# Kernel tuning notes

Hardware: AMD Instinct MI355X
Metric: run time of the kernel (lower is better)

Reference implementation:

```python
import jax, jax.numpy as jnp
import numpy as np

NEG = -1.0e9

def setup_inputs() -> dict:
    key = jax.random.key(0)
    k1, k2 = jax.random.split(key)
    B, S, D = 4, 4096, 256
    encodings = jax.random.normal(k1, (B, S, D), dtype=jnp.float32)
    # nn.Linear weight [out, in]; Linear applies x @ W.T
    W = jax.random.normal(k2, (D, D), dtype=jnp.float32) * (1.0 / np.sqrt(D))
    return {"encodings": encodings, "W": W}

def reference(encodings, W):
    B, S, D = encodings.shape
    enc_mult_W = jnp.einsum('bsd,ed->bse', encodings, W)          # Linear, no bias
    sims = jnp.einsum('bqd,bkd->bqk', encodings, enc_mult_W)       # E @ (EW^T)^T
    scaled = sims / jnp.asarray(np.sqrt(D), dtype=sims.dtype)
    # causal mask: positions k > q masked out (top-left softmax == 1)
    mask = jnp.triu(jnp.ones((S, S), dtype=bool), k=1)
    scaled = jnp.where(mask[None, :, :], jnp.asarray(NEG, scaled.dtype), scaled)
    attn = jax.nn.softmax(scaled, axis=-1)
    return jnp.einsum('bqk,bkd->bqd', attn, encodings)
```

## Files before the change

### kernel.cpp

```cpp
#include <hip/hip_runtime.h>
#include <hip/hip_bf16.h>
#include <cstdint>
#include <cstddef>

typedef __attribute__((ext_vector_type(4))) float f32x4;
typedef __attribute__((ext_vector_type(8))) short s16x8;
typedef __attribute__((ext_vector_type(4))) unsigned int u32x4;

#define SDIM 4096
#define DDIM 256

#define GLOAD_LDS16(g, s)                                                      \
  __builtin_amdgcn_global_load_lds(                                            \
      (const __attribute__((address_space(1))) void*)(g),                      \
      (__attribute__((address_space(3))) void*)(s), 16, 0, 0)

__device__ __forceinline__ unsigned short cvt_bf16(float f) {
  union { float f; unsigned int u; } v;
  v.f = f;
  unsigned int u = v.u;
  unsigned int r = (u + 0x7FFFu + ((u >> 16) & 1u)) >> 16;
  return (unsigned short)r;
}

__device__ __forceinline__ float bf2f(unsigned short s) {
  union { unsigned int u; float f; } v;
  v.u = ((unsigned int)s) << 16;
  return v.f;
}

__global__ __launch_bounds__(256) void k_convw(const float* __restrict__ W,
                                               unsigned short* __restrict__ Wb) {
  int i = (blockIdx.x * 256 + threadIdx.x) * 8;
  f32x4 a = *(const f32x4*)(W + i);
  f32x4 b = *(const f32x4*)(W + i + 4);
  s16x8 o;
#pragma unroll
  for (int j = 0; j < 4; ++j) {
    o[j] = (short)cvt_bf16(a[j]);
    o[4 + j] = (short)cvt_bf16(b[j]);
  }
  *(s16x8*)(Wb + i) = o;
}

__global__ __launch_bounds__(256) void k_transv(const float* __restrict__ E,
                                                unsigned short* __restrict__ Vt) {
  __shared__ float tile[64][65];
  const int tid = threadIdx.x;
  const int b = blockIdx.z;
  const int s0 = blockIdx.x * 64, d0 = blockIdx.y * 64;
  const int tx = tid & 63, ty = tid >> 6;
#pragma unroll
  for (int i = 0; i < 16; ++i) {
    int sr = i * 4 + ty;
    tile[sr][tx] = E[((size_t)(b * SDIM) + s0 + sr) * DDIM + d0 + tx];
  }
  __syncthreads();
#pragma unroll
  for (int i = 0; i < 16; ++i) {
    int dr = i * 4 + ty;
    Vt[((size_t)(b * DDIM) + d0 + dr) * SDIM + s0 + tx] = cvt_bf16(tile[tx][dr]);
  }
}

__global__ __launch_bounds__(256) void k_proj(const float* __restrict__ E,
                                              const unsigned short* __restrict__ Wb,
                                              unsigned short* __restrict__ Kp) {
  const int tid = threadIdx.x;
  const int w = tid >> 6, l = tid & 63, lhi = l >> 4, llo = l & 15;
  const int m0 = blockIdx.x * 64 + w * 16;
  f32x4 acc[16];
#pragma unroll
  for (int n = 0; n < 16; ++n) acc[n] = (f32x4){0.f, 0.f, 0.f, 0.f};
  const float* arow = E + (size_t)(m0 + llo) * DDIM;
#pragma unroll
  for (int kd = 0; kd < 8; ++kd) {
    const int dbase = kd * 32 + lhi * 8;
    f32x4 a0 = *(const f32x4*)(arow + dbase);
    f32x4 a1 = *(const f32x4*)(arow + dbase + 4);
    s16x8 af;
#pragma unroll
    for (int j = 0; j < 4; ++j) {
      af[j] = (short)cvt_bf16(a0[j]);
      af[4 + j] = (short)cvt_bf16(a1[j]);
    }
#pragma unroll
    for (int n = 0; n < 16; ++n) {
      s16x8 bf = *(const s16x8*)(Wb + (n * 16 + llo) * DDIM + dbase);
      acc[n] = __builtin_amdgcn_mfma_f32_16x16x32_bf16(af, bf, acc[n], 0, 0, 0);
    }
  }
  const float sc = 1.4426950408889634f / 16.0f;
#pragma unroll
  for (int n = 0; n < 16; ++n) {
#pragma unroll
    for (int r = 0; r < 4; ++r) {
      Kp[(size_t)(m0 + lhi * 4 + r) * DDIM + n * 16 + llo] = cvt_bf16(acc[n][r] * sc);
    }
  }
}

__global__ __launch_bounds__(256, 2) void k_attn(const float* __restrict__ E,
                                                 const unsigned short* __restrict__ Kp,
                                                 const unsigned short* __restrict__ Vt,
                                                 unsigned short* __restrict__ Po,
                                                 float* __restrict__ Lp, int nch) {
  __shared__ u32x4 smem4[4736];
  char* smem = (char*)smem4;
  const int tid = threadIdx.x;
  const int l = tid & 63, w = tid >> 6, lhi = l >> 4, llo = l & 15;
  const int u = blockIdx.x % (4 * nch);
  const int t_ = blockIdx.x / (4 * nch);
  const int qt = 31 - t_;
  const int b = u & 3, ch = u >> 2;
  const int q0 = qt * 128;
  const int chb = ch * 4 + b;
  const int nst = (4 * (qt + 1) - ch + nch - 1) / nch;
  const int wq0 = q0 + w * 32;

  if (4 * (qt + 1) <= ch) {
    char* Pz = (char*)(Po + ((size_t)chb * SDIM + q0) * DDIM);
    const u32x4 z = (u32x4){0u, 0u, 0u, 0u};
#pragma unroll
    for (int i = 0; i < 16; ++i) *(u32x4*)(Pz + tid * 256 + i * 16) = z;
    if (tid < 128) Lp[(size_t)chb * SDIM + q0 + tid] = 0.f;
    return;
  }

  s16x8 qf[2][8];
#pragma unroll
  for (int s = 0; s < 2; ++s) {
    const float* Eq = E + ((size_t)(b * SDIM) + wq0 + s * 16 + llo) * DDIM;
#pragma unroll
    for (int kd = 0; kd < 8; ++kd) {
      f32x4 a0 = *(const f32x4*)(Eq + kd * 32 + lhi * 8);
      f32x4 a1 = *(const f32x4*)(Eq + kd * 32 + lhi * 8 + 4);
#pragma unroll
      for (int j = 0; j < 4; ++j) {
        qf[s][kd][j] = (short)cvt_bf16(a0[j]);
        qf[s][kd][4 + j] = (short)cvt_bf16(a1[j]);
      }
    }
  }

  f32x4 oT[2][16];
#pragma unroll
  for (int s = 0; s < 2; ++s)
#pragma unroll
    for (int n = 0; n < 16; ++n) oT[s][n] = (f32x4){0.f, 0.f, 0.f, 0.f};
  float lsum[2] = {0.f, 0.f};

  const int trow = tid >> 5;
  const int kcolb = ((tid & 31) << 4) ^ ((trow & 7) << 4);
  const char* KpB = (const char*)Kp + (size_t)b * SDIM * 512;
  const char* VtB = (const char*)Vt + (size_t)b * DDIM * (SDIM * 2);
  const char* vsb = VtB + (size_t)(tid >> 2) * 8192 + (size_t)((tid & 3) * 8) * 2;

  auto stage = [&](int t) {
    const int kv0 = (ch + nch * t) * 32;
    char* kdst = smem + ((t & 1) * 16384);
    char* vdst = smem + 32768 + ((t & 1) * 16384);
    const char* ks = KpB + (size_t)(kv0 + trow) * 512 + kcolb;
    const char* vs = vsb + (size_t)kv0 * 2;
#pragma unroll
    for (int i = 0; i < 4; ++i)
      GLOAD_LDS16(ks + (size_t)i * 4096, kdst + i * 4096 + tid * 16);
#pragma unroll
    for (int i = 0; i < 4; ++i)
      GLOAD_LDS16(vs + (size_t)i * (64 * 8192), vdst + i * 4096 + tid * 16);
  };

  stage(0);
  char* sPw = smem + 65536 + w * 2560;

  for (int t = 0; t < nst; ++t) {
    const int kv0 = (ch + nch * t) * 32;
    const char* kb_ = smem + ((t & 1) * 16384);
    const char* vb_ = smem + 32768 + ((t & 1) * 16384);

    __syncthreads();
    if (t + 1 < nst) stage(t + 1);

#pragma unroll
    for (int kb = 0; kb < 2; ++kb) {
      f32x4 sa0 = (f32x4){0.f, 0.f, 0.f, 0.f};
      f32x4 sa1 = (f32x4){0.f, 0.f, 0.f, 0.f};
      const char* krow = kb_ + (kb * 16 + llo) * 512;
      __builtin_amdgcn_s_setprio(1);
#pragma unroll
      for (int kd = 0; kd < 8; ++kd) {
        s16x8 kf = *(const s16x8*)(krow + ((kd * 64 + lhi * 16) ^ ((llo & 7) << 4)));
        sa0 = __builtin_amdgcn_mfma_f32_16x16x32_bf16(kf, qf[0][kd], sa0, 0, 0, 0);
        sa1 = __builtin_amdgcn_mfma_f32_16x16x32_bf16(kf, qf[1][kd], sa1, 0, 0, 0);
      }
      __builtin_amdgcn_s_setprio(0);
      const int kvr = kv0 + kb * 16 + lhi * 4;
#pragma unroll
      for (int s = 0; s < 2; ++s) {
        const f32x4 sa = s ? sa1 : sa0;
        const int qi = wq0 + s * 16 + llo;
        float p[4];
#pragma unroll
        for (int rr = 0; rr < 4; ++rr) {
          float v = exp2f(sa[rr] - 32.0f);
          p[rr] = (kvr + rr > qi) ? 0.0f : v;
        }
        lsum[s] += (p[0] + p[1]) + (p[2] + p[3]);
        unsigned int w0 = __builtin_amdgcn_perm(__float_as_uint(p[1]),
                                                __float_as_uint(p[0]), 0x07060302u);
        unsigned int w1 = __builtin_amdgcn_perm(__float_as_uint(p[3]),
                                                __float_as_uint(p[2]), 0x07060302u);
        *(uint2*)(sPw + (s * 16 + llo) * 80 + kb * 32 + lhi * 8) = make_uint2(w0, w1);
      }
    }

    s16x8 pb0 = *(const s16x8*)(sPw + llo * 80 + lhi * 16);
    s16x8 pb1 = *(const s16x8*)(sPw + (16 + llo) * 80 + lhi * 16);
    __builtin_amdgcn_s_setprio(1);
#pragma unroll
    for (int n = 0; n < 16; ++n) {
      s16x8 vf = *(const s16x8*)(vb_ + (n * 16 + llo) * 64 + lhi * 16);
      oT[0][n] = __builtin_amdgcn_mfma_f32_16x16x32_bf16(vf, pb0, oT[0][n], 0, 0, 0);
      oT[1][n] = __builtin_amdgcn_mfma_f32_16x16x32_bf16(vf, pb1, oT[1][n], 0, 0, 0);
    }
    __builtin_amdgcn_s_setprio(0);
  }

#pragma unroll
  for (int s = 0; s < 2; ++s) {
    lsum[s] += __shfl_xor(lsum[s], 16);
    lsum[s] += __shfl_xor(lsum[s], 32);
  }
#pragma unroll
  for (int s = 0; s < 2; ++s) {
    const int q = wq0 + s * 16 + llo;
    unsigned short* PoW = Po + ((size_t)chb * SDIM + q) * DDIM;
#pragma unroll
    for (int n = 0; n < 16; ++n) {
      unsigned int w0 =
          (unsigned int)cvt_bf16(oT[s][n][0]) | ((unsigned int)cvt_bf16(oT[s][n][1]) << 16);
      unsigned int w1 =
          (unsigned int)cvt_bf16(oT[s][n][2]) | ((unsigned int)cvt_bf16(oT[s][n][3]) << 16);
      *(uint2*)(PoW + n * 16 + lhi * 4) = make_uint2(w0, w1);
    }
    if (lhi == 0) Lp[(size_t)chb * SDIM + q] = lsum[s];
  }
}

__global__ __launch_bounds__(256) void k_merge(const unsigned short* __restrict__ Po,
                                               const float* __restrict__ Lp,
                                               float* __restrict__ out, int nch) {
  const size_t e = ((size_t)blockIdx.x * 256 + threadIdx.x) * 8;
  const size_t f = e >> 8;
  float lt = 0.f;
  for (int c = 0; c < nch; ++c) lt += Lp[(size_t)c * 16384 + f];
  const float inv = 1.0f / lt;
  float acc[8] = {0.f, 0.f, 0.f, 0.f, 0.f, 0.f, 0.f, 0.f};
  for (int c = 0; c < nch; ++c) {
    s16x8 a = *(const s16x8*)(Po + (size_t)c * 4194304 + e);
#pragma unroll
    for (int j = 0; j < 8; ++j) acc[j] += bf2f((unsigned short)a[j]);
  }
  f32x4 o0, o1;
#pragma unroll
  for (int j = 0; j < 4; ++j) {
    o0[j] = acc[j] * inv;
    o1[j] = acc[4 + j] * inv;
  }
  *(f32x4*)(out + e) = o0;
  *(f32x4*)(out + e + 4) = o1;
}

extern "C" void kernel_launch(void* const* d_in, const int* in_sizes, int n_in,
                              void* d_out, int out_size, void* d_ws, size_t ws_size,
                              hipStream_t stream) {
  (void)in_sizes; (void)n_in; (void)out_size;
  const float* E = (const float*)d_in[0];
  const float* W = (const float*)d_in[1];
  float* out = (float*)d_out;
  char* ws = (char*)d_ws;

  const size_t base = 16777216ull;
  auto need = [&](int c) {
    return base + (size_t)c * 8388608ull + (size_t)c * 65536ull + 262144ull;
  };
  int nch = 2;
  if (ws_size >= need(8)) nch = 8;
  else if (ws_size >= need(4)) nch = 4;

  unsigned short* Kp = (unsigned short*)(ws);
  unsigned short* Vt = (unsigned short*)(ws + 8388608);
  unsigned short* Po = (unsigned short*)(ws + base);
  size_t lp_off = base + (size_t)nch * 8388608ull;
  float* Lp = (float*)(ws + lp_off);
  unsigned short* Wb = (unsigned short*)(ws + lp_off + (size_t)nch * 65536ull);

  k_convw<<<dim3(32), dim3(256), 0, stream>>>(W, Wb);
  k_transv<<<dim3(64, 4, 4), dim3(256), 0, stream>>>(E, Vt);
  k_proj<<<dim3(256), dim3(256), 0, stream>>>(E, Wb, Kp);
  k_attn<<<dim3(32 * 4 * nch), dim3(256), 0, stream>>>(E, Kp, Vt, Po, Lp, nch);
  k_merge<<<dim3(2048), dim3(256), 0, stream>>>(Po, Lp, out, nch);
}
```

Measured before the change: 126.3 us.

## Use 64-key tiles, read V from global, skip empty chunks, merge prep kernels

Fuses the W conversion and V transpose into one prep kernel, saving a launch. The attention kernel now processes 64-key tiles with only K staged through LDS, while V fragments are read directly from global memory. The P scratch layout is swizzled, and the causal mask is applied only on diagonal tiles. Chunks with no work return early instead of writing zeros, and the merge kernel sums only the chunks that could be valid. This cuts zero-fill traffic, merge reads and LDS traffic, at the cost of uncoalesced global V loads and bigger LDS use, which may lower occupancy.

```diff
diff --git a/kernel.cpp b/kernel.cpp
--- a/kernel.cpp
+++ b/kernel.cpp
@@ -29,26 +29,28 @@
   return v.f;
 }
 
-__global__ __launch_bounds__(256) void k_convw(const float* __restrict__ W,
-                                               unsigned short* __restrict__ Wb) {
-  int i = (blockIdx.x * 256 + threadIdx.x) * 8;
-  f32x4 a = *(const f32x4*)(W + i);
-  f32x4 b = *(const f32x4*)(W + i + 4);
-  s16x8 o;
-#pragma unroll
-  for (int j = 0; j < 4; ++j) {
-    o[j] = (short)cvt_bf16(a[j]);
-    o[4 + j] = (short)cvt_bf16(b[j]);
-  }
-  *(s16x8*)(Wb + i) = o;
-}
-
-__global__ __launch_bounds__(256) void k_transv(const float* __restrict__ E,
-                                                unsigned short* __restrict__ Vt) {
+__global__ __launch_bounds__(256) void k_prep(const float* __restrict__ E,
+                                              const float* __restrict__ W,
+                                              unsigned short* __restrict__ Wb,
+                                              unsigned short* __restrict__ Vt) {
   __shared__ float tile[64][65];
+  const int bid = blockIdx.x;
   const int tid = threadIdx.x;
-  const int b = blockIdx.z;
-  const int s0 = blockIdx.x * 64, d0 = blockIdx.y * 64;
+  if (bid >= 1024) {
+    int i = ((bid - 1024) * 256 + tid) * 8;
+    f32x4 a = *(const f32x4*)(W + i);
+    f32x4 b = *(const f32x4*)(W + i + 4);
+    s16x8 o;
+#pragma unroll
+    for (int j = 0; j < 4; ++j) {
+      o[j] = (short)cvt_bf16(a[j]);
+      o[4 + j] = (short)cvt_bf16(b[j]);
+    }
+    *(s16x8*)(Wb + i) = o;
+    return;
+  }
+  const int b = bid >> 8;
+  const int d0 = ((bid >> 6) & 3) * 64, s0 = (bid & 63) * 64;
   const int tx = tid & 63, ty = tid >> 6;
 #pragma unroll
   for (int i = 0; i < 16; ++i) {
@@ -105,7 +107,7 @@
                                                  const unsigned short* __restrict__ Vt,
                                                  unsigned short* __restrict__ Po,
                                                  float* __restrict__ Lp, int nch) {
-  __shared__ u32x4 smem4[4736];
+  __shared__ u32x4 smem4[5120];
   char* smem = (char*)smem4;
   const int tid = threadIdx.x;
   const int l = tid & 63, w = tid >> 6, lhi = l >> 4, llo = l & 15;
@@ -115,17 +117,10 @@
   const int b = u & 3, ch = u >> 2;
   const int q0 = qt * 128;
   const int chb = ch * 4 + b;
-  const int nst = (4 * (qt + 1) - ch + nch - 1) / nch;
+  const int ntile = 2 * (qt + 1);
+  if (ntile <= ch) return;
+  const int nst = (ntile - ch + nch - 1) / nch;
   const int wq0 = q0 + w * 32;
-
-  if (4 * (qt + 1) <= ch) {
-    char* Pz = (char*)(Po + ((size_t)chb * SDIM + q0) * DDIM);
-    const u32x4 z = (u32x4){0u, 0u, 0u, 0u};
-#pragma unroll
-    for (int i = 0; i < 16; ++i) *(u32x4*)(Pz + tid * 256 + i * 16) = z;
-    if (tid < 128) Lp[(size_t)chb * SDIM + q0 + tid] = 0.f;
-    return;
-  }
 
   s16x8 qf[2][8];
 #pragma unroll
@@ -154,35 +149,31 @@
   const int kcolb = ((tid & 31) << 4) ^ ((trow & 7) << 4);
   const char* KpB = (const char*)Kp + (size_t)b * SDIM * 512;
   const char* VtB = (const char*)Vt + (size_t)b * DDIM * (SDIM * 2);
-  const char* vsb = VtB + (size_t)(tid >> 2) * 8192 + (size_t)((tid & 3) * 8) * 2;
+  const char* vbase = VtB + (size_t)llo * 8192 + lhi * 16;
 
   auto stage = [&](int t) {
-    const int kv0 = (ch + nch * t) * 32;
-    char* kdst = smem + ((t & 1) * 16384);
-    char* vdst = smem + 32768 + ((t & 1) * 16384);
+    const int kv0 = (ch + nch * t) * 64;
+    char* kdst = smem + ((t & 1) * 32768);
     const char* ks = KpB + (size_t)(kv0 + trow) * 512 + kcolb;
-    const char* vs = vsb + (size_t)kv0 * 2;
-#pragma unroll
-    for (int i = 0; i < 4; ++i)
+#pragma unroll
+    for (int i = 0; i < 8; ++i)
       GLOAD_LDS16(ks + (size_t)i * 4096, kdst + i * 4096 + tid * 16);
-#pragma unroll
-    for (int i = 0; i < 4; ++i)
-      GLOAD_LDS16(vs + (size_t)i * (64 * 8192), vdst + i * 4096 + tid * 16);
   };
 
   stage(0);
-  char* sPw = smem + 65536 + w * 2560;
+  char* sPw = smem + 65536 + w * 4096;
+  const int prd = (llo & 3) << 5;
 
   for (int t = 0; t < nst; ++t) {
-    const int kv0 = (ch + nch * t) * 32;
-    const char* kb_ = smem + ((t & 1) * 16384);
-    const char* vb_ = smem + 32768 + ((t & 1) * 16384);
+    const int kv0 = (ch + nch * t) * 64;
+    const char* kb_ = smem + ((t & 1) * 32768);
 
     __syncthreads();
     if (t + 1 < nst) stage(t + 1);
 
-#pragma unroll
-    for (int kb = 0; kb < 2; ++kb) {
+    const bool diag = (kv0 + 64 > q0);
+#pragma unroll
+    for (int kb = 0; kb < 4; ++kb) {
       f32x4 sa0 = (f32x4){0.f, 0.f, 0.f, 0.f};
       f32x4 sa1 = (f32x4){0.f, 0.f, 0.f, 0.f};
       const char* krow = kb_ + (kb * 16 + llo) * 512;
@@ -198,30 +189,42 @@
 #pragma unroll
       for (int s = 0; s < 2; ++s) {
         const f32x4 sa = s ? sa1 : sa0;
-        const int qi = wq0 + s * 16 + llo;
         float p[4];
 #pragma unroll
-        for (int rr = 0; rr < 4; ++rr) {
-          float v = exp2f(sa[rr] - 32.0f);
-          p[rr] = (kvr + rr > qi) ? 0.0f : v;
+        for (int rr = 0; rr < 4; ++rr) p[rr] = exp2f(sa[rr] - 32.0f);
+        if (diag) {
+          const int qi = wq0 + s * 16 + llo;
+#pragma unroll
+          for (int rr = 0; rr < 4; ++rr)
+            if (kvr + rr > qi) p[rr] = 0.0f;
         }
         lsum[s] += (p[0] + p[1]) + (p[2] + p[3]);
         unsigned int w0 = __builtin_amdgcn_perm(__float_as_uint(p[1]),
                                                 __float_as_uint(p[0]), 0x07060302u);
         unsigned int w1 = __builtin_amdgcn_perm(__float_as_uint(p[3]),
                                                 __float_as_uint(p[2]), 0x07060302u);
-        *(uint2*)(sPw + (s * 16 + llo) * 80 + kb * 32 + lhi * 8) = make_uint2(w0, w1);
+        const int r = s * 16 + llo;
+        *(uint2*)(sPw + r * 128 + ((kb * 32 + lhi * 8) ^ ((r & 3) << 5))) =
+            make_uint2(w0, w1);
       }
     }
 
-    s16x8 pb0 = *(const s16x8*)(sPw + llo * 80 + lhi * 16);
-    s16x8 pb1 = *(const s16x8*)(sPw + (16 + llo) * 80 + lhi * 16);
+    s16x8 pb[2][2];
+#pragma unroll
+    for (int ks = 0; ks < 2; ++ks) {
+      pb[0][ks] = *(const s16x8*)(sPw + llo * 128 + ((ks * 64 + lhi * 16) ^ prd));
+      pb[1][ks] = *(const s16x8*)(sPw + (16 + llo) * 128 + ((ks * 64 + lhi * 16) ^ prd));
+    }
+    const char* vt0 = vbase + (size_t)kv0 * 2;
     __builtin_amdgcn_s_setprio(1);
 #pragma unroll
     for (int n = 0; n < 16; ++n) {
-      s16x8 vf = *(const s16x8*)(vb_ + (n * 16 + llo) * 64 + lhi * 16);
-      oT[0][n] = __builtin_amdgcn_mfma_f32_16x16x32_bf16(vf, pb0, oT[0][n], 0, 0, 0);
-      oT[1][n] = __builtin_amdgcn_mfma_f32_16x16x32_bf16(vf, pb1, oT[1][n], 0, 0, 0);
+#pragma unroll
+      for (int ks = 0; ks < 2; ++ks) {
+        s16x8 vf = *(const s16x8*)(vt0 + (size_t)n * 131072 + ks * 64);
+        oT[0][n] = __builtin_amdgcn_mfma_f32_16x16x32_bf16(vf, pb[0][ks], oT[0][n], 0, 0, 0);
+        oT[1][n] = __builtin_amdgcn_mfma_f32_16x16x32_bf16(vf, pb[1][ks], oT[1][n], 0, 0, 0);
+      }
     }
     __builtin_amdgcn_s_setprio(0);
   }
@@ -252,11 +255,13 @@
                                                float* __restrict__ out, int nch) {
   const size_t e = ((size_t)blockIdx.x * 256 + threadIdx.x) * 8;
   const size_t f = e >> 8;
+  const int s = (int)(f & 4095);
+  const int cnt = min(nch, 2 * (s >> 7) + 2);
   float lt = 0.f;
-  for (int c = 0; c < nch; ++c) lt += Lp[(size_t)c * 16384 + f];
+  for (int c = 0; c < cnt; ++c) lt += Lp[(size_t)c * 16384 + f];
   const float inv = 1.0f / lt;
   float acc[8] = {0.f, 0.f, 0.f, 0.f, 0.f, 0.f, 0.f, 0.f};
-  for (int c = 0; c < nch; ++c) {
+  for (int c = 0; c < cnt; ++c) {
     s16x8 a = *(const s16x8*)(Po + (size_t)c * 4194304 + e);
 #pragma unroll
     for (int j = 0; j < 8; ++j) acc[j] += bf2f((unsigned short)a[j]);
@@ -295,8 +300,7 @@
   float* Lp = (float*)(ws + lp_off);
   unsigned short* Wb = (unsigned short*)(ws + lp_off + (size_t)nch * 65536ull);
 
-  k_convw<<<dim3(32), dim3(256), 0, stream>>>(W, Wb);
-  k_transv<<<dim3(64, 4, 4), dim3(256), 0, stream>>>(E, Vt);
+  k_prep<<<dim3(1056), dim3(256), 0, stream>>>(E, W, Wb, Vt);
   k_proj<<<dim3(256), dim3(256), 0, stream>>>(E, Wb, Kp);
   k_attn<<<dim3(32 * 4 * nch), dim3(256), 0, stream>>>(E, Kp, Vt, Po, Lp, nch);
   k_merge<<<dim3(2048), dim3(256), 0, stream>>>(Po, Lp, out, nch);
```

Result: slower. 192.3 us (+52.3%).

## Pair causal q-tiles per block, fuse prep kernels, skip empty chunks in merge

Applied to the files above, without the earlier changes.

Each attention block now handles two query tiles, p and 31-p, so every block gets a similar amount of causal work and the grid halves. Blocks no longer zero-fill Po and Lp for chunks with no valid keys. The merge kernel instead sums only the chunks that can hold data for each row. The W conversion and V transpose kernels are merged into one launch to save a kernel launch. In exchange, fewer blocks are in flight and each block runs longer and serially, which may reduce latency hiding.

```diff
diff --git a/kernel.cpp b/kernel.cpp
--- a/kernel.cpp
+++ b/kernel.cpp
@@ -29,26 +29,28 @@
   return v.f;
 }
 
-__global__ __launch_bounds__(256) void k_convw(const float* __restrict__ W,
-                                               unsigned short* __restrict__ Wb) {
-  int i = (blockIdx.x * 256 + threadIdx.x) * 8;
-  f32x4 a = *(const f32x4*)(W + i);
-  f32x4 b = *(const f32x4*)(W + i + 4);
-  s16x8 o;
-#pragma unroll
-  for (int j = 0; j < 4; ++j) {
-    o[j] = (short)cvt_bf16(a[j]);
-    o[4 + j] = (short)cvt_bf16(b[j]);
-  }
-  *(s16x8*)(Wb + i) = o;
-}
-
-__global__ __launch_bounds__(256) void k_transv(const float* __restrict__ E,
-                                                unsigned short* __restrict__ Vt) {
+__global__ __launch_bounds__(256) void k_prep(const float* __restrict__ E,
+                                              const float* __restrict__ W,
+                                              unsigned short* __restrict__ Wb,
+                                              unsigned short* __restrict__ Vt) {
   __shared__ float tile[64][65];
+  const int bid = blockIdx.x;
   const int tid = threadIdx.x;
-  const int b = blockIdx.z;
-  const int s0 = blockIdx.x * 64, d0 = blockIdx.y * 64;
+  if (bid >= 1024) {
+    int i = ((bid - 1024) * 256 + tid) * 8;
+    f32x4 a = *(const f32x4*)(W + i);
+    f32x4 b = *(const f32x4*)(W + i + 4);
+    s16x8 o;
+#pragma unroll
+    for (int j = 0; j < 4; ++j) {
+      o[j] = (short)cvt_bf16(a[j]);
+      o[4 + j] = (short)cvt_bf16(b[j]);
+    }
+    *(s16x8*)(Wb + i) = o;
+    return;
+  }
+  const int b = bid >> 8;
+  const int d0 = ((bid >> 6) & 3) * 64, s0 = (bid & 63) * 64;
   const int tx = tid & 63, ty = tid >> 6;
 #pragma unroll
   for (int i = 0; i < 16; ++i) {
@@ -110,140 +112,138 @@
   const int tid = threadIdx.x;
   const int l = tid & 63, w = tid >> 6, lhi = l >> 4, llo = l & 15;
   const int u = blockIdx.x % (4 * nch);
-  const int t_ = blockIdx.x / (4 * nch);
-  const int qt = 31 - t_;
+  const int p = blockIdx.x / (4 * nch);
   const int b = u & 3, ch = u >> 2;
-  const int q0 = qt * 128;
   const int chb = ch * 4 + b;
-  const int nst = (4 * (qt + 1) - ch + nch - 1) / nch;
-  const int wq0 = q0 + w * 32;
-
-  if (4 * (qt + 1) <= ch) {
-    char* Pz = (char*)(Po + ((size_t)chb * SDIM + q0) * DDIM);
-    const u32x4 z = (u32x4){0u, 0u, 0u, 0u};
-#pragma unroll
-    for (int i = 0; i < 16; ++i) *(u32x4*)(Pz + tid * 256 + i * 16) = z;
-    if (tid < 128) Lp[(size_t)chb * SDIM + q0 + tid] = 0.f;
-    return;
-  }
-
-  s16x8 qf[2][8];
-#pragma unroll
-  for (int s = 0; s < 2; ++s) {
-    const float* Eq = E + ((size_t)(b * SDIM) + wq0 + s * 16 + llo) * DDIM;
-#pragma unroll
-    for (int kd = 0; kd < 8; ++kd) {
-      f32x4 a0 = *(const f32x4*)(Eq + kd * 32 + lhi * 8);
-      f32x4 a1 = *(const f32x4*)(Eq + kd * 32 + lhi * 8 + 4);
-#pragma unroll
-      for (int j = 0; j < 4; ++j) {
-        qf[s][kd][j] = (short)cvt_bf16(a0[j]);
-        qf[s][kd][4 + j] = (short)cvt_bf16(a1[j]);
-      }
-    }
-  }
-
-  f32x4 oT[2][16];
-#pragma unroll
-  for (int s = 0; s < 2; ++s)
-#pragma unroll
-    for (int n = 0; n < 16; ++n) oT[s][n] = (f32x4){0.f, 0.f, 0.f, 0.f};
-  float lsum[2] = {0.f, 0.f};
 
   const int trow = tid >> 5;
   const int kcolb = ((tid & 31) << 4) ^ ((trow & 7) << 4);
   const char* KpB = (const char*)Kp + (size_t)b * SDIM * 512;
   const char* VtB = (const char*)Vt + (size_t)b * DDIM * (SDIM * 2);
   const char* vsb = VtB + (size_t)(tid >> 2) * 8192 + (size_t)((tid & 3) * 8) * 2;
-
-  auto stage = [&](int t) {
-    const int kv0 = (ch + nch * t) * 32;
-    char* kdst = smem + ((t & 1) * 16384);
-    char* vdst = smem + 32768 + ((t & 1) * 16384);
-    const char* ks = KpB + (size_t)(kv0 + trow) * 512 + kcolb;
-    const char* vs = vsb + (size_t)kv0 * 2;
-#pragma unroll
-    for (int i = 0; i < 4; ++i)
-      GLOAD_LDS16(ks + (size_t)i * 4096, kdst + i * 4096 + tid * 16);
-#pragma unroll
-    for (int i = 0; i < 4; ++i)
-      GLOAD_LDS16(vs + (size_t)i * (64 * 8192), vdst + i * 4096 + tid * 16);
-  };
-
-  stage(0);
   char* sPw = smem + 65536 + w * 2560;
 
-  for (int t = 0; t < nst; ++t) {
-    const int kv0 = (ch + nch * t) * 32;
-    const char* kb_ = smem + ((t & 1) * 16384);
-    const char* vb_ = smem + 32768 + ((t & 1) * 16384);
-
-    __syncthreads();
-    if (t + 1 < nst) stage(t + 1);
-
-#pragma unroll
-    for (int kb = 0; kb < 2; ++kb) {
-      f32x4 sa0 = (f32x4){0.f, 0.f, 0.f, 0.f};
-      f32x4 sa1 = (f32x4){0.f, 0.f, 0.f, 0.f};
-      const char* krow = kb_ + (kb * 16 + llo) * 512;
+  for (int c2 = 0; c2 < 2; ++c2) {
+    const int qt = c2 ? (31 - p) : p;
+    const int q0 = qt * 128;
+    const int ntile = 4 * (qt + 1);
+    if (ntile <= ch) continue;
+    const int nst = (ntile - ch + nch - 1) / nch;
+    const int wq0 = q0 + w * 32;
+
+    if (c2) __syncthreads();
+
+    s16x8 qf[2][8];
+#pragma unroll
+    for (int s = 0; s < 2; ++s) {
+      const float* Eq = E + ((size_t)(b * SDIM) + wq0 + s * 16 + llo) * DDIM;
+#pragma unroll
+      for (int kd = 0; kd < 8; ++kd) {
+        f32x4 a0 = *(const f32x4*)(Eq + kd * 32 + lhi * 8);
+        f32x4 a1 = *(const f32x4*)(Eq + kd * 32 + lhi * 8 + 4);
+#pragma unroll
+        for (int j = 0; j < 4; ++j) {
+          qf[s][kd][j] = (short)cvt_bf16(a0[j]);
+          qf[s][kd][4 + j] = (short)cvt_bf16(a1[j]);
+        }
+      }
+    }
+
+    f32x4 oT[2][16];
+#pragma unroll
+    for (int s = 0; s < 2; ++s)
+#pragma unroll
+      for (int n = 0; n < 16; ++n) oT[s][n] = (f32x4){0.f, 0.f, 0.f, 0.f};
+    float lsum[2] = {0.f, 0.f};
+
+    auto stage = [&](int t) {
+      const int kv0 = (ch + nch * t) * 32;
+      char* kdst = smem + ((t & 1) * 16384);
+      char* vdst = smem + 32768 + ((t & 1) * 16384);
+      const char* ks = KpB + (size_t)(kv0 + trow) * 512 + kcolb;
+      const char* vs = vsb + (size_t)kv0 * 2;
+#pragma unroll
+      for (int i = 0; i < 4; ++i)
+        GLOAD_LDS16(ks + (size_t)i * 4096, kdst + i * 4096 + tid * 16);
+#pragma unroll
+      for (int i = 0; i < 4; ++i)
+        GLOAD_LDS16(vs + (size_t)i * (64 * 8192), vdst + i * 4096 + tid * 16);
+    };
+
+    stage(0);
+
+    for (int t = 0; t < nst; ++t) {
+      const int kv0 = (ch + nch * t) * 32;
+      const char* kb_ = smem + ((t & 1) * 16384);
+      const char* vb_ = smem + 32768 + ((t & 1) * 16384);
+
+      __syncthreads();
+      if (t + 1 < nst) stage(t + 1);
+
+#pragma unroll
+      for (int kb = 0; kb < 2; ++kb) {
+        f32x4 sa0 = (f32x4){0.f, 0.f, 0.f, 0.f};
+        f32x4 sa1 = (f32x4){0.f, 0.f, 0.f, 0.f};
+        const char* krow = kb_ + (kb * 16 + llo) * 512;
+        __builtin_amdgcn_s_setprio(1);
+#pragma unroll
+        for (int kd = 0; kd < 8; ++kd) {
+          s16x8 kf = *(const s16x8*)(krow + ((kd * 64 + lhi * 16) ^ ((llo & 7) << 4)));
+          sa0 = __builtin_amdgcn_mfma_f32_16x16x32_bf16(kf, qf[0][kd], sa0, 0, 0, 0);
+          sa1 = __builtin_amdgcn_mfma_f32_16x16x32_bf16(kf, qf[1][kd], sa1, 0, 0, 0);
+        }
+        __builtin_amdgcn_s_setprio(0);
+        const int kvr = kv0 + kb * 16 + lhi * 4;
+#pragma unroll
+        for (int s = 0; s < 2; ++s) {
+          const f32x4 sa = s ? sa1 : sa0;
+          const int qi = wq0 + s * 16 + llo;
+          float pv[4];
+#pragma unroll
+          for (int rr = 0; rr < 4; ++rr) {
+            float v = exp2f(sa[rr] - 32.0f);
+            pv[rr] = (kvr + rr > qi) ? 0.0f : v;
+          }
+          lsum[s] += (pv[0] + pv[1]) + (pv[2] + pv[3]);
+          unsigned int w0 = __builtin_amdgcn_perm(__float_as_uint(pv[1]),
+                                                  __float_as_uint(pv[0]), 0x07060302u);
+          unsigned int w1 = __builtin_amdgcn_perm(__float_as_uint(pv[3]),
+                                                  __float_as_uint(pv[2]), 0x07060302u);
+          *(uint2*)(sPw + (s * 16 + llo) * 80 + kb * 32 + lhi * 8) = make_uint2(w0, w1);
+        }
+      }
+
+      s16x8 pb0 = *(const s16x8*)(sPw + llo * 80 + lhi * 16);
+      s16x8 pb1 = *(const s16x8*)(sPw + (16 + llo) * 80 + lhi * 16);
       __builtin_amdgcn_s_setprio(1);
 #pragma unroll
-      for (int kd = 0; kd < 8; ++kd) {
-        s16x8 kf = *(const s16x8*)(krow + ((kd * 64 + lhi * 16) ^ ((llo & 7) << 4)));
-        sa0 = __builtin_amdgcn_mfma_f32_16x16x32_bf16(kf, qf[0][kd], sa0, 0, 0, 0);
-        sa1 = __builtin_amdgcn_mfma_f32_16x16x32_bf16(kf, qf[1][kd], sa1, 0, 0, 0);
+      for (int n = 0; n < 16; ++n) {
+        s16x8 vf = *(const s16x8*)(vb_ + (n * 16 + llo) * 64 + lhi * 16);
+        oT[0][n] = __builtin_amdgcn_mfma_f32_16x16x32_bf16(vf, pb0, oT[0][n], 0, 0, 0);
+        oT[1][n] = __builtin_amdgcn_mfma_f32_16x16x32_bf16(vf, pb1, oT[1][n], 0, 0, 0);
       }
       __builtin_amdgcn_s_setprio(0);
-      const int kvr = kv0 + kb * 16 + lhi * 4;
-#pragma unroll
-      for (int s = 0; s < 2; ++s) {
-        const f32x4 sa = s ? sa1 : sa0;
-        const int qi = wq0 + s * 16 + llo;
-        float p[4];
-#pragma unroll
-        for (int rr = 0; rr < 4; ++rr) {
-          float v = exp2f(sa[rr] - 32.0f);
-          p[rr] = (kvr + rr > qi) ? 0.0f : v;
-        }
-        lsum[s] += (p[0] + p[1]) + (p[2] + p[3]);
-        unsigned int w0 = __builtin_amdgcn_perm(__float_as_uint(p[1]),
-                                                __float_as_uint(p[0]), 0x07060302u);
-        unsigned int w1 = __builtin_amdgcn_perm(__float_as_uint(p[3]),
-                                                __float_as_uint(p[2]), 0x07060302u);
-        *(uint2*)(sPw + (s * 16 + llo) * 80 + kb * 32 + lhi * 8) = make_uint2(w0, w1);
+    }
+
+#pragma unroll
+    for (int s = 0; s < 2; ++s) {
+      lsum[s] += __shfl_xor(lsum[s], 16);
+      lsum[s] += __shfl_xor(lsum[s], 32);
+    }
+#pragma unroll
+    for (int s = 0; s < 2; ++s) {
+      const int q = wq0 + s * 16 + llo;
+      unsigned short* PoW = Po + ((size_t)chb * SDIM + q) * DDIM;
+#pragma unroll
+      for (int n = 0; n < 16; ++n) {
+        unsigned int w0 = (unsigned int)cvt_bf16(oT[s][n][0]) |
+                          ((unsigned int)cvt_bf16(oT[s][n][1]) << 16);
+        unsigned int w1 = (unsigned int)cvt_bf16(oT[s][n][2]) |
+                          ((unsigned int)cvt_bf16(oT[s][n][3]) << 16);
+        *(uint2*)(PoW + n * 16 + lhi * 4) = make_uint2(w0, w1);
       }
-    }
-
-    s16x8 pb0 = *(const s16x8*)(sPw + llo * 80 + lhi * 16);
-    s16x8 pb1 = *(const s16x8*)(sPw + (16 + llo) * 80 + lhi * 16);
-    __builtin_amdgcn_s_setprio(1);
-#pragma unroll
-    for (int n = 0; n < 16; ++n) {
-      s16x8 vf = *(const s16x8*)(vb_ + (n * 16 + llo) * 64 + lhi * 16);
-      oT[0][n] = __builtin_amdgcn_mfma_f32_16x16x32_bf16(vf, pb0, oT[0][n], 0, 0, 0);
-      oT[1][n] = __builtin_amdgcn_mfma_f32_16x16x32_bf16(vf, pb1, oT[1][n], 0, 0, 0);
-    }
-    __builtin_amdgcn_s_setprio(0);
-  }
-
-#pragma unroll
-  for (int s = 0; s < 2; ++s) {
-    lsum[s] += __shfl_xor(lsum[s], 16);
-    lsum[s] += __shfl_xor(lsum[s], 32);
-  }
-#pragma unroll
-  for (int s = 0; s < 2; ++s) {
-    const int q = wq0 + s * 16 + llo;
-    unsigned short* PoW = Po + ((size_t)chb * SDIM + q) * DDIM;
-#pragma unroll
-    for (int n = 0; n < 16; ++n) {
-      unsigned int w0 =
-          (unsigned int)cvt_bf16(oT[s][n][0]) | ((unsigned int)cvt_bf16(oT[s][n][1]) << 16);
-      unsigned int w1 =
-          (unsigned int)cvt_bf16(oT[s][n][2]) | ((unsigned int)cvt_bf16(oT[s][n][3]) << 16);
-      *(uint2*)(PoW + n * 16 + lhi * 4) = make_uint2(w0, w1);
-    }
-    if (lhi == 0) Lp[(size_t)chb * SDIM + q] = lsum[s];
+      if (lhi == 0) Lp[(size_t)chb * SDIM + q] = lsum[s];
+    }
   }
 }
 
@@ -252,11 +252,13 @@
                                                float* __restrict__ out, int nch) {
   const size_t e = ((size_t)blockIdx.x * 256 + threadIdx.x) * 8;
   const size_t f = e >> 8;
+  const int s = (int)(f & 4095);
+  const int cnt = min(nch, 4 * (s >> 7) + 4);
   float lt = 0.f;
-  for (int c = 0; c < nch; ++c) lt += Lp[(size_t)c * 16384 + f];
+  for (int c = 0; c < cnt; ++c) lt += Lp[(size_t)c * 16384 + f];
   const float inv = 1.0f / lt;
   float acc[8] = {0.f, 0.f, 0.f, 0.f, 0.f, 0.f, 0.f, 0.f};
-  for (int c = 0; c < nch; ++c) {
+  for (int c = 0; c < cnt; ++c) {
     s16x8 a = *(const s16x8*)(Po + (size_t)c * 4194304 + e);
 #pragma unroll
     for (int j = 0; j < 8; ++j) acc[j] += bf2f((unsigned short)a[j]);
@@ -295,9 +297,8 @@
   float* Lp = (float*)(ws + lp_off);
   unsigned short* Wb = (unsigned short*)(ws + lp_off + (size_t)nch * 65536ull);
 
-  k_convw<<<dim3(32), dim3(256), 0, stream>>>(W, Wb);
-  k_transv<<<dim3(64, 4, 4), dim3(256), 0, stream>>>(E, Vt);
+  k_prep<<<dim3(1056), dim3(256), 0, stream>>>(E, W, Wb, Vt);
   k_proj<<<dim3(256), dim3(256), 0, stream>>>(E, Wb, Kp);
-  k_attn<<<dim3(32 * 4 * nch), dim3(256), 0, stream>>>(E, Kp, Vt, Po, Lp, nch);
+  k_attn<<<dim3(16 * 4 * nch), dim3(256), 0, stream>>>(E, Kp, Vt, Po, Lp, nch);
   k_merge<<<dim3(2048), dim3(256), 0, stream>>>(Po, Lp, out, nch);
 }
```

Measured after the change: 128.5 us. Within noise of the previous version (+1.7%).
